# Kernel tuning notes

Hardware: AMD Instinct MI355X
Metric: run time of the kernel (lower is better)

The kernel has to match this reference:

```python
import jax, jax.numpy as jnp
import numpy as np


def setup_inputs() -> dict:
    key = jax.random.key(0)
    k1, k2 = jax.random.split(key)
    # bilateral grid: [N, grid_h, grid_w, grid_d, C]
    grid = jax.random.normal(k1, (4, 16, 16, 8, 12), dtype=jnp.float32)
    # guide map in [0, 1]: [N, H, W]
    guide = jax.random.uniform(k2, (4, 1024, 1024), dtype=jnp.float32)
    return {"grid": grid, "guide": guide}


def reference(grid, guide):
    """HDRNet bilateral_slice: per-pixel trilinear interpolation into the
    bilateral grid, with z coordinate given by the guide map.

    grid:  [N, gh, gw, gd, C]
    guide: [N, H, W] in [0, 1]
    out:   [N, H, W, C]
    """
    N, gh, gw, gd, C = grid.shape
    _, H, W = guide.shape

    # continuous grid coordinates (pixel centers)
    gx = (jnp.arange(W, dtype=guide.dtype) + 0.5) * (gw / W)   # [W]
    gy = (jnp.arange(H, dtype=guide.dtype) + 0.5) * (gh / H)   # [H]
    gz = guide * gd                                            # [N, H, W]

    fx = jnp.floor(gx - 0.5)
    fy = jnp.floor(gy - 0.5)
    fz = jnp.floor(gz - 0.5)

    batch = jnp.arange(N)[:, None, None]                       # [N, 1, 1]
    out = jnp.zeros((N, H, W, C), dtype=grid.dtype)

    # 8 trilinear corners (2 taps per axis, tent weights, clamped indices)
    for i in (0, 1):
        xx = fx + i
        wx = jnp.maximum(1.0 - jnp.abs(xx + 0.5 - gx), 0.0)    # [W]
        cx = jnp.clip(xx, 0, gw - 1).astype(jnp.int32)
        for j in (0, 1):
            yy = fy + j
            wy = jnp.maximum(1.0 - jnp.abs(yy + 0.5 - gy), 0.0)  # [H]
            cy = jnp.clip(yy, 0, gh - 1).astype(jnp.int32)
            for k in (0, 1):
                zz = fz + k
                wz = jnp.maximum(1.0 - jnp.abs(zz + 0.5 - gz), 0.0)  # [N,H,W]
                cz = jnp.clip(zz, 0, gd - 1).astype(jnp.int32)
                # gather corner values: [N, H, W, C]
                vals = grid[batch, cy[None, :, None], cx[None, None, :], cz]
                w = (wy[None, :, None] * wx[None, None, :] * wz)[..., None]
                out = out + w * vals
    return out
```

## Files before the change

kernel.cpp:

```cpp
#include <hip/hip_runtime.h>


#define GH 16
#define GW 16
#define GD 8
#define NC 12
#define IMH 1024
#define IMW 1024
#define NBATCH 4

__device__ __forceinline__ void fma4(float4& a, float w, const float4& v) {
    a.x = fmaf(w, v.x, a.x);
    a.y = fmaf(w, v.y, a.y);
    a.z = fmaf(w, v.z, a.z);
    a.w = fmaf(w, v.w, a.w);
}

__global__ __launch_bounds__(256) void bilateral_slice_kernel(
    const float* __restrict__ grid,
    const float* __restrict__ guide,
    float* __restrict__ out)
{
    __shared__ float4 lds4[3 * 256];

    const int t = threadIdx.x;
    const int idx = blockIdx.x * 256 + t;
    const int x = idx & (IMW - 1);
    const int y = (idx >> 10) & (IMH - 1);
    const int n = idx >> 20;

    const float gx = (x + 0.5f) * ((float)GW / (float)IMW);
    const float gy = (y + 0.5f) * ((float)GH / (float)IMH);
    const float gz = guide[idx] * (float)GD;

    const float fx = floorf(gx - 0.5f);
    const float fy = floorf(gy - 0.5f);
    const float fz = floorf(gz - 0.5f);

    float wx[2], wy[2], wz[2];
    int cx[2], cy[2], cz[2];
#pragma unroll
    for (int i = 0; i < 2; ++i) {
        const float xx = fx + (float)i;
        const float yy = fy + (float)i;
        const float zz = fz + (float)i;
        wx[i] = fmaxf(1.0f - fabsf(xx + 0.5f - gx), 0.0f);
        wy[i] = fmaxf(1.0f - fabsf(yy + 0.5f - gy), 0.0f);
        wz[i] = fmaxf(1.0f - fabsf(zz + 0.5f - gz), 0.0f);
        cx[i] = min(max((int)xx, 0), GW - 1);
        cy[i] = min(max((int)yy, 0), GH - 1);
        cz[i] = min(max((int)zz, 0), GD - 1);
    }

    float4 a0 = make_float4(0.f, 0.f, 0.f, 0.f);
    float4 a1 = make_float4(0.f, 0.f, 0.f, 0.f);
    float4 a2 = make_float4(0.f, 0.f, 0.f, 0.f);

    const float* gbase = grid + (size_t)n * (GH * GW * GD * NC);
#pragma unroll
    for (int j = 0; j < 2; ++j) {
#pragma unroll
        for (int i = 0; i < 2; ++i) {
            const float wxy = wy[j] * wx[i];
            const float* gp = gbase + (cy[j] * GW + cx[i]) * (GD * NC);
#pragma unroll
            for (int k = 0; k < 2; ++k) {
                const float w = wxy * wz[k];
                const float4* g4 = (const float4*)(gp + cz[k] * NC);
                const float4 v0 = g4[0];
                const float4 v1 = g4[1];
                const float4 v2 = g4[2];
                fma4(a0, w, v0);
                fma4(a1, w, v1);
                fma4(a2, w, v2);
            }
        }
    }

    lds4[0 * 256 + t] = a0;
    lds4[1 * 256 + t] = a1;
    lds4[2 * 256 + t] = a2;
    __syncthreads();

    float4* __restrict__ out4 = (float4*)out + (size_t)blockIdx.x * 768;
#pragma unroll
    for (int s = 0; s < 3; ++s) {
        const int e = s * 256 + t;
        const int p = e / 3;
        const int part = e - 3 * p;
        out4[e] = lds4[part * 256 + p];
    }
}

extern "C" void kernel_launch(void* const* d_in, const int* in_sizes, int n_in,
                              void* d_out, int out_size, void* d_ws, size_t ws_size,
                              hipStream_t stream) {
    const float* grid  = (const float*)d_in[0];
    const float* guide = (const float*)d_in[1];
    float* out = (float*)d_out;

    const int total_pixels = NBATCH * IMH * IMW;
    const int block = 256;
    const int nblocks = total_pixels / block;

    bilateral_slice_kernel<<<nblocks, block, 0, stream>>>(grid, guide, out);
}
```

Before: 248.5 us.

## Stage the two needed grid rows in LDS and store outputs directly with nontemporal writes

Each block covers a quarter of one image row, so it only ever reads two grid rows. Both rows (2x1536 floats) are now copied cooperatively into LDS and the eight trilinear gathers read from LDS, replacing scattered global/L2 gathers. The LDS transpose used for coalesced output is dropped. Each thread instead writes its 48 bytes directly with nontemporal stores, which adds strided per-thread stores in exchange for removing one barrier pass and the LDS staging of results. The index math and the float4 arithmetic are also reworked to use ext_vector types.

```diff
diff --git a/kernel.cpp b/kernel.cpp
--- a/kernel.cpp
+++ b/kernel.cpp
@@ -8,12 +8,14 @@
 #define IMH 1024
 #define IMW 1024
 #define NBATCH 4
+#define ROW_FLOATS (GW * GD * NC)
+#define CELL_DW   (GD * NC)
+#define Z_DW      (NC)
 
-__device__ __forceinline__ void fma4(float4& a, float w, const float4& v) {
-    a.x = fmaf(w, v.x, a.x);
-    a.y = fmaf(w, v.y, a.y);
-    a.z = fmaf(w, v.z, a.z);
-    a.w = fmaf(w, v.w, a.w);
+typedef float f32x4 __attribute__((ext_vector_type(4)));
+
+__device__ __forceinline__ void fma4(f32x4& a, float w, const f32x4& v) {
+    a = a + w * v;
 }
 
 __global__ __launch_bounds__(256) void bilateral_slice_kernel(
@@ -21,7 +23,7 @@
     const float* __restrict__ guide,
     float* __restrict__ out)
 {
-    __shared__ float4 lds4[3 * 256];
+    __shared__ float rowlds[2 * ROW_FLOATS];
 
     const int t = threadIdx.x;
     const int idx = blockIdx.x * 256 + t;
@@ -29,47 +31,64 @@
     const int y = (idx >> 10) & (IMH - 1);
     const int n = idx >> 20;
 
+    const float gy = (y + 0.5f) * ((float)GH / (float)IMH);
+    const float fy = floorf(gy - 0.5f);
+    const int fyi = (int)fy;
+    const int cy0 = min(max(fyi, 0), GH - 1);
+    const int cy1 = min(max(fyi + 1, 0), GH - 1);
+    float wy[2];
+    wy[0] = fmaxf(1.0f - fabsf(fy + 0.5f - gy), 0.0f);
+    wy[1] = fmaxf(1.0f - fabsf(fy + 1.5f - gy), 0.0f);
+
+    const float* gbase = grid + (size_t)n * (GH * ROW_FLOATS);
+    const f32x4* src0 = (const f32x4*)(gbase + cy0 * ROW_FLOATS);
+    const f32x4* src1 = (const f32x4*)(gbase + cy1 * ROW_FLOATS);
+    f32x4* dst = (f32x4*)rowlds;
+#pragma unroll
+    for (int s = 0; s < 3; ++s) {
+        const int f = s * 256 + t;
+        const int rs = (f >= 384) ? 1 : 0;
+        const f32x4* src = rs ? src1 : src0;
+        dst[f] = src[f - rs * 384];
+    }
+
     const float gx = (x + 0.5f) * ((float)GW / (float)IMW);
-    const float gy = (y + 0.5f) * ((float)GH / (float)IMH);
     const float gz = guide[idx] * (float)GD;
 
     const float fx = floorf(gx - 0.5f);
-    const float fy = floorf(gy - 0.5f);
     const float fz = floorf(gz - 0.5f);
 
-    float wx[2], wy[2], wz[2];
-    int cx[2], cy[2], cz[2];
+    float wx[2], wz[2];
+    int cx[2], cz[2];
 #pragma unroll
     for (int i = 0; i < 2; ++i) {
         const float xx = fx + (float)i;
-        const float yy = fy + (float)i;
         const float zz = fz + (float)i;
         wx[i] = fmaxf(1.0f - fabsf(xx + 0.5f - gx), 0.0f);
-        wy[i] = fmaxf(1.0f - fabsf(yy + 0.5f - gy), 0.0f);
         wz[i] = fmaxf(1.0f - fabsf(zz + 0.5f - gz), 0.0f);
-        cx[i] = min(max((int)xx, 0), GW - 1);
-        cy[i] = min(max((int)yy, 0), GH - 1);
-        cz[i] = min(max((int)zz, 0), GD - 1);
+        cx[i] = min(max((int)fx + i, 0), GW - 1);
+        cz[i] = min(max((int)fz + i, 0), GD - 1);
     }
 
-    float4 a0 = make_float4(0.f, 0.f, 0.f, 0.f);
-    float4 a1 = make_float4(0.f, 0.f, 0.f, 0.f);
-    float4 a2 = make_float4(0.f, 0.f, 0.f, 0.f);
+    __syncthreads();
 
-    const float* gbase = grid + (size_t)n * (GH * GW * GD * NC);
+    f32x4 a0 = (f32x4)0.f;
+    f32x4 a1 = (f32x4)0.f;
+    f32x4 a2 = (f32x4)0.f;
+
 #pragma unroll
     for (int j = 0; j < 2; ++j) {
 #pragma unroll
         for (int i = 0; i < 2; ++i) {
             const float wxy = wy[j] * wx[i];
-            const float* gp = gbase + (cy[j] * GW + cx[i]) * (GD * NC);
+            const int cellbase = j * ROW_FLOATS + cx[i] * CELL_DW;
 #pragma unroll
             for (int k = 0; k < 2; ++k) {
                 const float w = wxy * wz[k];
-                const float4* g4 = (const float4*)(gp + cz[k] * NC);
-                const float4 v0 = g4[0];
-                const float4 v1 = g4[1];
-                const float4 v2 = g4[2];
+                const f32x4* g4 = (const f32x4*)&rowlds[cellbase + cz[k] * Z_DW];
+                const f32x4 v0 = g4[0];
+                const f32x4 v1 = g4[1];
+                const f32x4 v2 = g4[2];
                 fma4(a0, w, v0);
                 fma4(a1, w, v1);
                 fma4(a2, w, v2);
@@ -77,19 +96,10 @@
         }
     }
 
-    lds4[0 * 256 + t] = a0;
-    lds4[1 * 256 + t] = a1;
-    lds4[2 * 256 + t] = a2;
-    __syncthreads();
-
-    float4* __restrict__ out4 = (float4*)out + (size_t)blockIdx.x * 768;
-#pragma unroll
-    for (int s = 0; s < 3; ++s) {
-        const int e = s * 256 + t;
-        const int p = e / 3;
-        const int part = e - 3 * p;
-        out4[e] = lds4[part * 256 + p];
-    }
+    f32x4* o = (f32x4*)(out + (size_t)idx * NC);
+    __builtin_nontemporal_store(a0, o + 0);
+    __builtin_nontemporal_store(a1, o + 1);
+    __builtin_nontemporal_store(a2, o + 2);
 }
 
 extern "C" void kernel_launch(void* const* d_in, const int* in_sizes, int n_in,
```

Measured after the change: 269.5 us. +8.5%, slower.
